# Kernel tuning notes

Hardware: AMD Instinct MI355X
Metric: run time of the kernel (lower is better)

The kernel has to match this reference:

```python
import jax, jax.numpy as jnp
import numpy as np

INPUT_SIZE = 1024
HIDDEN = [2048, 2048]
OUTPUT_SIZE = 10
N = 16384
PRIOR_VAR = 100.0


def setup_inputs() -> dict:
    key = jax.random.key(0)
    ks = jax.random.split(key, 8)
    X = jax.random.normal(ks[0], (N, INPUT_SIZE), dtype=jnp.float32)
    Y = jax.random.randint(ks[1], (N,), 0, OUTPUT_SIZE, dtype=jnp.int32)
    # Kaiming-ish init like nn.Linear defaults (scale irrelevant to correctness)
    def lin(k, fan_in, fan_out):
        bound = 1.0 / np.sqrt(fan_in)
        kw, kb = jax.random.split(k)
        W = jax.random.uniform(kw, (fan_out, fan_in), jnp.float32, -bound, bound)
        b = jax.random.uniform(kb, (fan_out,), jnp.float32, -bound, bound)
        return W, b
    W1, b1 = lin(ks[2], INPUT_SIZE, HIDDEN[0])
    W2, b2 = lin(ks[3], HIDDEN[0], HIDDEN[1])
    W3, b3 = lin(ks[4], HIDDEN[1], OUTPUT_SIZE)
    return {"X": X, "Y": Y, "W1": W1, "b1": b1, "W2": W2, "b2": b2, "W3": W3, "b3": b3}


def reference(X, Y, W1, b1, W2, b2, W3, b3):
    # Batched version of the per-sample Linear+ReLU+...+Linear+Softmax(dim=0) loop.
    h = jax.nn.relu(X @ W1.T + b1)            # [N, H0]
    h = jax.nn.relu(h @ W2.T + b2)            # [N, H1]
    logits = h @ W3.T + b3                    # [N, C]
    # Categorical(probs=softmax(logits)).log_prob(Y[i]) == log_softmax(logits)[i, Y[i]]
    logp = jax.nn.log_softmax(logits, axis=-1)
    log_likelihood = jnp.sum(jnp.take_along_axis(logp, Y[:, None].astype(jnp.int32), axis=-1))
    # MVN(0, 100*I) log-prob over flattened params: closed-form diagonal Gaussian.
    params = (W1, b1, W2, b2, W3, b3)
    d = sum(p.size for p in params)
    sq = sum(jnp.sum(p * p) for p in params)
    log_prior = -0.5 * (sq / PRIOR_VAR + d * jnp.log(2.0 * jnp.pi * PRIOR_VAR))
    return log_likelihood + log_prior
```

## Files before the change

kernel.cpp:

```cpp
#include <hip/hip_runtime.h>
#include <math.h>

typedef __bf16 bf16;
typedef bf16 bf16x8 __attribute__((ext_vector_type(8)));
typedef bf16 bf16x4 __attribute__((ext_vector_type(4)));
typedef float f32x4 __attribute__((ext_vector_type(4)));

#define NROWS 16384
#define HID 2048

__global__ __launch_bounds__(256) void cvt_kernel(const float* __restrict__ src,
                                                  bf16* __restrict__ dst, int n4) {
  int stride = gridDim.x * blockDim.x;
  for (int i = blockIdx.x * blockDim.x + threadIdx.x; i < n4; i += stride) {
    float4 v = ((const float4*)src)[i];
    bf16x4 o;
    o[0] = (bf16)v.x; o[1] = (bf16)v.y; o[2] = (bf16)v.z; o[3] = (bf16)v.w;
    ((bf16x4*)dst)[i] = o;
  }
}

__device__ __forceinline__ void gload_lds16(const bf16* g, bf16* l) {
  __builtin_amdgcn_global_load_lds((const __attribute__((address_space(1))) void*)g,
                                   (__attribute__((address_space(3))) void*)l,
                                   16, 0, 0);
}

template <bool RELU>
__global__ __launch_bounds__(256) void gemm_bt(const bf16* __restrict__ A,
                                               const bf16* __restrict__ B,
                                               const float* __restrict__ bias,
                                               bf16* __restrict__ C,
                                               int M, int N, int K) {
  __shared__ bf16 Asub[128 * 32];
  __shared__ bf16 Bsub[128 * 32];
  const int tid = threadIdx.x;
  const int lane = tid & 63;
  const int w = tid >> 6;
  const int wr = w >> 1, wc = w & 1;
  const int bm = blockIdx.x, bn = blockIdx.y;
  const size_t baseA = (size_t)bm * 128 * K;
  const size_t baseB = (size_t)bn * 128 * K;

  f32x4 acc[4][4] = {};

  const int srow = lane >> 2;
  const int scol = (lane & 3) * 8;

  for (int k0 = 0; k0 < K; k0 += 32) {
#pragma unroll
    for (int i = 0; i < 2; ++i) {
      const int chunk = i * 4 + w;
      const int row = chunk * 16 + srow;
      gload_lds16(A + baseA + (size_t)row * K + k0 + scol, &Asub[chunk * 512]);
      gload_lds16(B + baseB + (size_t)row * K + k0 + scol, &Bsub[chunk * 512]);
    }
    __syncthreads();

    bf16x8 a[4], b[4];
#pragma unroll
    for (int mi = 0; mi < 4; ++mi)
      a[mi] = *(const bf16x8*)&Asub[(wr * 64 + mi * 16 + (lane & 15)) * 32 + (lane >> 4) * 8];
#pragma unroll
    for (int ni = 0; ni < 4; ++ni)
      b[ni] = *(const bf16x8*)&Bsub[(wc * 64 + ni * 16 + (lane & 15)) * 32 + (lane >> 4) * 8];
#pragma unroll
    for (int mi = 0; mi < 4; ++mi)
#pragma unroll
      for (int ni = 0; ni < 4; ++ni)
        acc[mi][ni] = __builtin_amdgcn_mfma_f32_16x16x32_bf16(a[mi], b[ni], acc[mi][ni], 0, 0, 0);
    __syncthreads();
  }

  const int crow0 = bm * 128 + wr * 64 + (lane >> 4) * 4;
  const int ccol0 = bn * 128 + wc * 64 + (lane & 15);
#pragma unroll
  for (int mi = 0; mi < 4; ++mi) {
#pragma unroll
    for (int ni = 0; ni < 4; ++ni) {
      const int col = ccol0 + ni * 16;
      const float bv = bias[col];
#pragma unroll
      for (int j = 0; j < 4; ++j) {
        const int row = crow0 + mi * 16 + j;
        float v = acc[mi][ni][j] + bv;
        if (RELU) v = fmaxf(v, 0.f);
        C[(size_t)row * N + col] = (bf16)v;
      }
    }
  }
}

__global__ __launch_bounds__(256) void loss_kernel(const bf16* __restrict__ h2,
                                                   const bf16* __restrict__ W3b,
                                                   const float* __restrict__ b3,
                                                   const int* __restrict__ Y,
                                                   float* __restrict__ acc) {
  __shared__ bf16 w3s[10 * HID];
  for (int i = threadIdx.x; i < 10 * HID / 8; i += 256)
    ((bf16x8*)w3s)[i] = ((const bf16x8*)W3b)[i];
  __syncthreads();

  const int lane = threadIdx.x & 63;
  const int w = threadIdx.x >> 6;
  const int nwave = gridDim.x * 4;
  float lsum = 0.f;

  for (int row = blockIdx.x * 4 + w; row < NROWS; row += nwave) {
    float p[10];
#pragma unroll
    for (int c = 0; c < 10; ++c) p[c] = 0.f;
    const bf16* hrow = h2 + (size_t)row * HID;
#pragma unroll
    for (int it = 0; it < 4; ++it) {
      const int k = it * 512 + lane * 8;
      bf16x8 hv = *(const bf16x8*)&hrow[k];
      float hf[8];
#pragma unroll
      for (int j = 0; j < 8; ++j) hf[j] = (float)hv[j];
#pragma unroll
      for (int c = 0; c < 10; ++c) {
        bf16x8 wv = *(const bf16x8*)&w3s[c * HID + k];
        float dp = 0.f;
#pragma unroll
        for (int j = 0; j < 8; ++j) dp += hf[j] * (float)wv[j];
        p[c] += dp;
      }
    }
#pragma unroll
    for (int off = 32; off; off >>= 1)
#pragma unroll
      for (int c = 0; c < 10; ++c) p[c] += __shfl_xor(p[c], off, 64);

    float lg[10], m = -1e30f;
#pragma unroll
    for (int c = 0; c < 10; ++c) { lg[c] = p[c] + b3[c]; m = fmaxf(m, lg[c]); }
    float s = 0.f;
#pragma unroll
    for (int c = 0; c < 10; ++c) s += expf(lg[c] - m);
    const float lse = m + logf(s);
    const int y = Y[row];
    float ly = 0.f;
#pragma unroll
    for (int c = 0; c < 10; ++c) ly += (c == y) ? lg[c] : 0.f;
    lsum += ly - lse;
  }
  if (lane == 0) atomicAdd(&acc[0], lsum);
}

struct SqArgs { const float* p[6]; int n[6]; };

__global__ __launch_bounds__(256) void sumsq_kernel(SqArgs args, float* __restrict__ acc) {
  float s = 0.f;
  const int stride = gridDim.x * blockDim.x;
  for (int a = 0; a < 6; ++a) {
    const float* p = args.p[a];
    const int n = args.n[a];
    for (int i = blockIdx.x * blockDim.x + threadIdx.x; i < n; i += stride) {
      float v = p[i];
      s += v * v;
    }
  }
#pragma unroll
  for (int off = 32; off; off >>= 1) s += __shfl_xor(s, off, 64);
  if ((threadIdx.x & 63) == 0) atomicAdd(&acc[1], s);
}

__global__ void finalize_kernel(float* __restrict__ out, const float* __restrict__ acc,
                                double dterm) {
  out[0] = (float)((double)acc[0] - 0.5 * ((double)acc[1] / 100.0 + dterm));
}

extern "C" void kernel_launch(void* const* d_in, const int* in_sizes, int n_in,
                              void* d_out, int out_size, void* d_ws, size_t ws_size,
                              hipStream_t stream) {
  const float* X  = (const float*)d_in[0];
  const int*   Y  = (const int*)d_in[1];
  const float* W1 = (const float*)d_in[2];
  const float* b1 = (const float*)d_in[3];
  const float* W2 = (const float*)d_in[4];
  const float* b2 = (const float*)d_in[5];
  const float* W3 = (const float*)d_in[6];
  const float* b3 = (const float*)d_in[7];
  float* out = (float*)d_out;

  char* ws = (char*)d_ws;
  size_t off = 0;
  auto alloc = [&](size_t bytes) -> void* {
    void* p = ws + off;
    off += (bytes + 255) & ~(size_t)255;
    return p;
  };
  bf16* Xb  = (bf16*)alloc((size_t)NROWS * 1024 * 2);
  bf16* W1b = (bf16*)alloc((size_t)HID * 1024 * 2);
  bf16* W2b = (bf16*)alloc((size_t)HID * HID * 2);
  bf16* W3b = (bf16*)alloc((size_t)10 * HID * 2);
  bf16* h1  = (bf16*)alloc((size_t)NROWS * HID * 2);
  bf16* h2  = (bf16*)alloc((size_t)NROWS * HID * 2);
  float* acc = (float*)alloc(256);

  hipMemsetAsync(acc, 0, 16, stream);

  auto cvt = [&](const float* s, bf16* d, int n) {
    int n4 = n / 4;
    int grid = (n4 + 255) / 256;
    if (grid > 4096) grid = 4096;
    cvt_kernel<<<grid, 256, 0, stream>>>(s, d, n4);
  };
  cvt(X,  Xb,  NROWS * 1024);
  cvt(W1, W1b, HID * 1024);
  cvt(W2, W2b, HID * HID);
  cvt(W3, W3b, 10 * HID);

  SqArgs sq;
  sq.p[0] = W1; sq.n[0] = in_sizes[2];
  sq.p[1] = b1; sq.n[1] = in_sizes[3];
  sq.p[2] = W2; sq.n[2] = in_sizes[4];
  sq.p[3] = b2; sq.n[3] = in_sizes[5];
  sq.p[4] = W3; sq.n[4] = in_sizes[6];
  sq.p[5] = b3; sq.n[5] = in_sizes[7];
  sumsq_kernel<<<512, 256, 0, stream>>>(sq, acc);

  gemm_bt<true><<<dim3(NROWS / 128, HID / 128), 256, 0, stream>>>(
      Xb, W1b, b1, h1, NROWS, HID, 1024);
  gemm_bt<true><<<dim3(NROWS / 128, HID / 128), 256, 0, stream>>>(
      h1, W2b, b2, h2, NROWS, HID, HID);

  loss_kernel<<<256, 256, 0, stream>>>(h2, W3b, b3, Y, acc);

  long long d = 0;
  for (int i = 2; i < 8; ++i) d += in_sizes[i];
  double dterm = (double)d * log(2.0 * M_PI * 100.0);
  finalize_kernel<<<1, 1, 0, stream>>>(out, acc, dterm);
}
```

Baseline: 505.7 us.

## Rewrite GEMM with 256x256 tiles, 4-stage LDS pipeline, swizzle and block remap

```diff
diff --git a/kernel.cpp b/kernel.cpp
--- a/kernel.cpp
+++ b/kernel.cpp
@@ -26,56 +26,95 @@
                                    16, 0, 0);
 }
 
-template <bool RELU>
-__global__ __launch_bounds__(256) void gemm_bt(const bf16* __restrict__ A,
+template <int K, bool RELU>
+__global__ __launch_bounds__(512) void gemm256(const bf16* __restrict__ A,
                                                const bf16* __restrict__ B,
                                                const float* __restrict__ bias,
-                                               bf16* __restrict__ C,
-                                               int M, int N, int K) {
-  __shared__ bf16 Asub[128 * 32];
-  __shared__ bf16 Bsub[128 * 32];
+                                               bf16* __restrict__ C, int N) {
+  extern __shared__ bf16 smem[];
+  constexpr int NT = K / 32;
   const int tid = threadIdx.x;
   const int lane = tid & 63;
   const int w = tid >> 6;
-  const int wr = w >> 1, wc = w & 1;
-  const int bm = blockIdx.x, bn = blockIdx.y;
-  const size_t baseA = (size_t)bm * 128 * K;
-  const size_t baseB = (size_t)bn * 128 * K;
-
-  f32x4 acc[4][4] = {};
-
-  const int srow = lane >> 2;
-  const int scol = (lane & 3) * 8;
-
-  for (int k0 = 0; k0 < K; k0 += 32) {
-#pragma unroll
-    for (int i = 0; i < 2; ++i) {
-      const int chunk = i * 4 + w;
-      const int row = chunk * 16 + srow;
-      gload_lds16(A + baseA + (size_t)row * K + k0 + scol, &Asub[chunk * 512]);
-      gload_lds16(B + baseB + (size_t)row * K + k0 + scol, &Bsub[chunk * 512]);
-    }
-    __syncthreads();
-
-    bf16x8 a[4], b[4];
-#pragma unroll
-    for (int mi = 0; mi < 4; ++mi)
-      a[mi] = *(const bf16x8*)&Asub[(wr * 64 + mi * 16 + (lane & 15)) * 32 + (lane >> 4) * 8];
-#pragma unroll
-    for (int ni = 0; ni < 4; ++ni)
-      b[ni] = *(const bf16x8*)&Bsub[(wc * 64 + ni * 16 + (lane & 15)) * 32 + (lane >> 4) * 8];
-#pragma unroll
-    for (int mi = 0; mi < 4; ++mi)
+  const int wr = w >> 2, wc = w & 3;
+
+  const int c = blockIdx.x & 7, l = blockIdx.x >> 3;
+  const int bm = c * 8 + (l >> 3);
+  const int bn = l & 7;
+
+  const bf16* Abase = A + (size_t)bm * 256 * K;
+  const bf16* Bbase = B + (size_t)bn * 256 * K;
+
+  const int r0 = tid >> 2;
+  const int r1 = r0 + 128;
+  const int kp = tid & 3;
+  const size_t offS0 = (size_t)r0 * K + ((kp ^ ((r0 >> 1) & 3)) * 8);
+  const size_t offS1 = (size_t)r1 * K + ((kp ^ ((r1 >> 1) & 3)) * 8);
+
+  int offRA[8], offRB[4];
+  const int kk = lane >> 4;
+#pragma unroll
+  for (int mi = 0; mi < 8; ++mi) {
+    const int r = wr * 128 + mi * 16 + (lane & 15);
+    offRA[mi] = (r * 4 + (kk ^ ((r >> 1) & 3))) * 8;
+  }
+#pragma unroll
+  for (int ni = 0; ni < 4; ++ni) {
+    const int r = wc * 64 + ni * 16 + (lane & 15);
+    offRB[ni] = (r * 4 + (kk ^ ((r >> 1) & 3))) * 8 + 8192;
+  }
+
+  f32x4 acc[8][4] = {};
+
+#define STAGE(t, b)                                                   \
+  {                                                                   \
+    const bf16* As = Abase + (size_t)(t) * 32;                        \
+    const bf16* Bs = Bbase + (size_t)(t) * 32;                        \
+    bf16* d = smem + (b) * 16384 + w * 512;    \
+    gload_lds16(As + offS0, d);                                       \
+    gload_lds16(As + offS1, d + 4096);                                \
+    gload_lds16(Bs + offS0, d + 8192);                                \
+    gload_lds16(Bs + offS1, d + 12288);                               \
+  }
+
+  STAGE(0, 0); STAGE(1, 1); STAGE(2, 2);
+  asm volatile("s_waitcnt vmcnt(8)" ::: "memory");
+  __builtin_amdgcn_s_barrier();
+  asm volatile("" ::: "memory");
+
+  for (int t = 0; t < NT; ++t) {
+    if (t + 3 < NT) STAGE(t + 3, (t + 3) & 3);
+
+    const bf16* base = smem + (t & 3) * 16384;
+    bf16x8 af[8], bfr[4];
+#pragma unroll
+    for (int mi = 0; mi < 8; ++mi) af[mi] = *(const bf16x8*)(base + offRA[mi]);
+#pragma unroll
+    for (int ni = 0; ni < 4; ++ni) bfr[ni] = *(const bf16x8*)(base + offRB[ni]);
+
+    __builtin_amdgcn_s_setprio(1);
+#pragma unroll
+    for (int mi = 0; mi < 8; ++mi)
 #pragma unroll
       for (int ni = 0; ni < 4; ++ni)
-        acc[mi][ni] = __builtin_amdgcn_mfma_f32_16x16x32_bf16(a[mi], b[ni], acc[mi][ni], 0, 0, 0);
-    __syncthreads();
-  }
-
-  const int crow0 = bm * 128 + wr * 64 + (lane >> 4) * 4;
-  const int ccol0 = bn * 128 + wc * 64 + (lane & 15);
-#pragma unroll
-  for (int mi = 0; mi < 4; ++mi) {
+        acc[mi][ni] = __builtin_amdgcn_mfma_f32_16x16x32_bf16(af[mi], bfr[ni], acc[mi][ni], 0, 0, 0);
+    __builtin_amdgcn_s_setprio(0);
+    asm volatile("" ::: "memory");
+
+    if (t + 1 < NT) {
+      if (t + 3 < NT)      asm volatile("s_waitcnt vmcnt(8)" ::: "memory");
+      else if (t + 2 < NT) asm volatile("s_waitcnt vmcnt(4)" ::: "memory");
+      else                 asm volatile("s_waitcnt vmcnt(0)" ::: "memory");
+      __builtin_amdgcn_s_barrier();
+      asm volatile("" ::: "memory");
+    }
+  }
+#undef STAGE
+
+  const int crow0 = bm * 256 + wr * 128 + (lane >> 4) * 4;
+  const int ccol0 = bn * 256 + wc * 64 + (lane & 15);
+#pragma unroll
+  for (int mi = 0; mi < 8; ++mi) {
 #pragma unroll
     for (int ni = 0; ni < 4; ++ni) {
       const int col = ccol0 + ni * 16;
@@ -221,10 +260,13 @@
   sq.p[5] = b3; sq.n[5] = in_sizes[7];
   sumsq_kernel<<<512, 256, 0, stream>>>(sq, acc);
 
-  gemm_bt<true><<<dim3(NROWS / 128, HID / 128), 256, 0, stream>>>(
-      Xb, W1b, b1, h1, NROWS, HID, 1024);
-  gemm_bt<true><<<dim3(NROWS / 128, HID / 128), 256, 0, stream>>>(
-      h1, W2b, b2, h2, NROWS, HID, HID);
+  hipFuncSetAttribute((const void*)gemm256<1024, true>,
+                      hipFuncAttributeMaxDynamicSharedMemorySize, 131072);
+  hipFuncSetAttribute((const void*)gemm256<2048, true>,
+                      hipFuncAttributeMaxDynamicSharedMemorySize, 131072);
+
+  gemm256<1024, true><<<512, 512, 131072, stream>>>(Xb, W1b, b1, h1, HID);
+  gemm256<2048, true><<<512, 512, 131072, stream>>>(h1, W2b, b2, h2, HID);
 
   loss_kernel<<<256, 256, 0, stream>>>(h2, W3b, b3, Y, acc);
 
```

Measured after the change: 436.7 us. 13.6% less time.
